# Kernel optimization log

Hardware: AMD Instinct MI355X
Metric: run time of the kernel (lower is better)

The kernel has to match this reference:

```python
import jax, jax.numpy as jnp
import numpy as np

DIM = 384
K = 64               # num_classes
TEMP = 0.1
BASE_TEMP = 2.0
LAMB = 25.0
PIXEL_SIZE = 50      # pixel_update_freq * 5
K_BAN = 10
SINKHORN_ITERS = 3
BS, N = 16, 512


def _l2norm(x, eps=1e-12):
    return x / jnp.maximum(jnp.linalg.norm(x, axis=-1, keepdims=True), eps)


def _online_clustering(scores):
    # SwAV-style Sinkhorn in log space on lamb-scaled cosine logits, then argmax.
    logq = scores
    for _ in range(SINKHORN_ITERS):
        logq = logq - jax.scipy.special.logsumexp(logq, axis=1, keepdims=True)
        logq = logq - jax.scipy.special.logsumexp(logq, axis=0, keepdims=True)
    return jnp.argmax(logq, axis=1)


def _supcon(anchor, y_anchor, contrast, y_contrast, exclude_diag, require_pos):
    # mask[i,j] = 1 if same label
    mask = (y_anchor[:, None] == y_contrast[None, :]).astype(anchor.dtype)
    logits = (anchor @ contrast.T) / TEMP
    logits = logits - jax.lax.stop_gradient(jnp.max(logits, axis=1, keepdims=True))
    if exclude_diag:
        mask = mask * (1.0 - jnp.eye(anchor.shape[0], dtype=anchor.dtype))
    exp_logits = jnp.exp(logits)
    # note: neg_mask = 1 - mask, so for exclude_diag the self term counts as negative (faithful)
    neg = (exp_logits * (1.0 - mask)).sum(axis=1, keepdims=True)
    log_prob = logits - jnp.log(exp_logits + neg)
    pos_cnt = mask.sum(axis=1)
    num = (mask * log_prob).sum(axis=1)
    if require_pos:
        valid = (pos_cnt > 0).astype(anchor.dtype)
        mlpp = jnp.where(pos_cnt > 0, num / jnp.maximum(pos_cnt, 1.0), 0.0)
        return -(TEMP / BASE_TEMP) * jnp.sum(mlpp) / jnp.maximum(valid.sum(), 1.0)
    return jnp.mean(-(TEMP / BASE_TEMP) * num / pos_cnt)


def _forward(feats, off_feats, cluster_center, point_queue):
    bs, n, dim = off_feats.shape
    n_off = _l2norm(off_feats.reshape(-1, dim))
    cluster_feats = jnp.concatenate([n_off, point_queue.reshape(-1, dim)], axis=0)
    log_alpha = cluster_feats @ cluster_center.T              # (bs*n + K*PIXEL_SIZE, K)
    labels = _online_clustering(log_alpha * LAMB)[: bs * n]
    f = _l2norm(feats).reshape(-1, dim)
    # ppc2: anchors vs sampled queue entries (same random column indices for every class)
    k_samp = PIXEL_SIZE - K_BAN
    idx = jax.random.permutation(jax.random.key(1), PIXEL_SIZE)[:k_samp]
    x_c = point_queue[:, idx, :].reshape(-1, dim)             # (K*k_samp, dim)
    y_c = jnp.repeat(jnp.arange(K), k_samp)
    loss = _supcon(f, labels, x_c, y_c, exclude_diag=False, require_pos=False)
    # ppc: anchors vs anchors, diagonal removed from positives
    loss = loss + _supcon(f, labels, f, labels, exclude_diag=True, require_pos=True)
    return loss


def setup_inputs() -> dict:
    key = jax.random.key(0)
    k1, k2, k3, k4 = jax.random.split(key, 4)
    feats = jax.random.normal(k1, (BS, N, DIM), dtype=jnp.float32)
    off_feats = jax.random.normal(k2, (BS, N, DIM), dtype=jnp.float32)
    cluster_center = _l2norm(jax.random.normal(k3, (K, DIM), dtype=jnp.float32))
    point_queue = _l2norm(jax.random.normal(k4, (K, PIXEL_SIZE, DIM), dtype=jnp.float32))
    return {"feats": feats, "off_feats": off_feats,
            "cluster_center": cluster_center, "point_queue": point_queue}


def reference(feats, off_feats, cluster_center, point_queue):
    return _forward(feats, off_feats, cluster_center, point_queue)
```

## Files before the change

### kernel.cpp

```cpp
#include <hip/hip_runtime.h>
#include <stdint.h>
#include <algorithm>

#define DIM   384
#define KCLS  64
#define NPIX  50
#define KSAMP 40
#define NANCH 8192
#define NQ    3200
#define NTOT  11392
#define NXC   2560

typedef __attribute__((ext_vector_type(8)))  short s16x8;
typedef __attribute__((ext_vector_type(16))) float f32x16;

struct Idx40 { int v[KSAMP]; };

__device__ __forceinline__ float wave_sum64(float v){
  #pragma unroll
  for (int o = 32; o >= 1; o >>= 1) v += __shfl_xor(v, o);
  return v;
}

__device__ __forceinline__ unsigned short f2bf(float x){
  union { float f; uint32_t u; } c; c.f = x;
  uint32_t r = c.u + 0x7FFFu + ((c.u >> 16) & 1u);
  if ((c.u & 0x7F800000u) == 0x7F800000u) r = c.u;
  return (unsigned short)(r >> 16);
}

__device__ __forceinline__ float bf2f(unsigned short h){
  union { uint32_t u; float f; } c; c.u = ((uint32_t)h) << 16;
  return c.f;
}

__device__ __forceinline__ void split_hl(float x, unsigned short& hi, unsigned short& lo){
  hi = f2bf(x);
  lo = f2bf(x - bf2f(hi));
}

__device__ __forceinline__ void gload16(const unsigned short* g, unsigned short* l){
  __builtin_amdgcn_global_load_lds(
      (const __attribute__((address_space(1))) unsigned int*)g,
      (__attribute__((address_space(3))) unsigned int*)l, 16, 0, 0);
}

__global__ __launch_bounds__(256) void norm_copy_k(const float* __restrict__ feats,
    const float* __restrict__ off, const float* __restrict__ pq,
    const float* __restrict__ CC,
    unsigned short* __restrict__ fNh,
    unsigned short* __restrict__ CFhi, unsigned short* __restrict__ CFlo,
    unsigned short* __restrict__ cchi, unsigned short* __restrict__ cclo,
    unsigned short* __restrict__ xch, Idx40 idx){
  int row  = blockIdx.x * 4 + (threadIdx.x >> 6);
  int lane = threadIdx.x & 63;
  if (row < 2 * NANCH){
    const float* src = (row < NANCH) ? feats + (size_t)row * DIM
                                     : off + (size_t)(row - NANCH) * DIM;
    float v[6]; float ss = 0.f;
    #pragma unroll
    for (int e = 0; e < 6; e++){ v[e] = src[lane + 64 * e]; ss += v[e] * v[e]; }
    ss = wave_sum64(ss);
    float inv = 1.f / fmaxf(sqrtf(ss), 1e-12f);
    if (row < NANCH){
      unsigned short* dh = fNh + (size_t)row * DIM;
      #pragma unroll
      for (int e = 0; e < 6; e++) dh[lane + 64 * e] = f2bf(v[e] * inv);
    } else {
      size_t base = (size_t)(row - NANCH) * DIM;
      #pragma unroll
      for (int e = 0; e < 6; e++){
        unsigned short h, l;
        split_hl(v[e] * inv, h, l);
        CFhi[base + lane + 64 * e] = h;
        CFlo[base + lane + 64 * e] = l;
      }
    }
  } else if (row < 2 * NANCH + NQ){
    int q = row - 2 * NANCH;
    const float* src = pq + (size_t)q * DIM;
    size_t base = (size_t)(NANCH + q) * DIM;
    #pragma unroll
    for (int e = 0; e < 6; e++){
      unsigned short h, l;
      split_hl(src[lane + 64 * e], h, l);
      CFhi[base + lane + 64 * e] = h;
      CFlo[base + lane + 64 * e] = l;
    }
  } else if (row < 2 * NANCH + NQ + KCLS){
    int r = row - 2 * NANCH - NQ;
    size_t base = (size_t)r * DIM;
    #pragma unroll
    for (int e = 0; e < 6; e++){
      unsigned short h, l;
      split_hl(CC[base + lane + 64 * e], h, l);
      cchi[base + lane + 64 * e] = h;
      cclo[base + lane + 64 * e] = l;
    }
  } else {
    int q = row - 2 * NANCH - NQ - KCLS;
    int c = q / KSAMP, t = q - c * KSAMP;
    const float* src = pq + ((size_t)c * NPIX + idx.v[t]) * DIM;
    unsigned short* dst = xch + (size_t)q * DIM;
    #pragma unroll
    for (int e = 0; e < 6; e++) dst[lane + 64 * e] = f2bf(src[lane + 64 * e]);
  }
}

__global__ __launch_bounds__(256) void gemm_logq_mfma_k(
    const unsigned short* __restrict__ Ahi, const unsigned short* __restrict__ Alo,
    const unsigned short* __restrict__ Bhi, const unsigned short* __restrict__ Blo,
    float* __restrict__ logq){
  __shared__ unsigned short lAh[128 * 64], lAl[128 * 64];
  __shared__ unsigned short lBh[64 * 64],  lBl[64 * 64];
  int t = threadIdx.x;
  int lane = t & 63, w = t >> 6;
  int l31 = lane & 31, half = lane >> 5;
  int i0 = blockIdx.x * 128;

  int rA = w * 32 + l31;
  int swA = ((rA & 7) << 4);
  int rB0 = l31, rB1 = 32 + l31;
  int swB = ((l31 & 7) << 4);

  f32x16 acc0, acc1;
  #pragma unroll
  for (int r = 0; r < 16; r++){ acc0[r] = 0.f; acc1[r] = 0.f; }

  for (int kc = 0; kc < 6; kc++){
    __syncthreads();
    #pragma unroll
    for (int p = 0; p < 4; p++){
      int c = t + p * 256;
      int row = c >> 3, col = c & 7;
      int sw = ((col << 4) ^ ((row & 7) << 4));
      *(s16x8*)((char*)lAh + row * 128 + sw) =
          *(const s16x8*)(Ahi + (size_t)(i0 + row) * DIM + kc * 64 + col * 8);
      *(s16x8*)((char*)lAl + row * 128 + sw) =
          *(const s16x8*)(Alo + (size_t)(i0 + row) * DIM + kc * 64 + col * 8);
    }
    #pragma unroll
    for (int p = 0; p < 2; p++){
      int c = t + p * 256;
      int row = c >> 3, col = c & 7;
      int sw = ((col << 4) ^ ((row & 7) << 4));
      *(s16x8*)((char*)lBh + row * 128 + sw) =
          *(const s16x8*)(Bhi + (size_t)row * DIM + kc * 64 + col * 8);
      *(s16x8*)((char*)lBl + row * 128 + sw) =
          *(const s16x8*)(Blo + (size_t)row * DIM + kc * 64 + col * 8);
    }
    __syncthreads();
    #pragma unroll
    for (int kk = 0; kk < 4; kk++){
      int kb = kk * 32 + half * 16;
      s16x8 fah  = *(const s16x8*)((char*)lAh + rA * 128 + (kb ^ swA));
      s16x8 fal  = *(const s16x8*)((char*)lAl + rA * 128 + (kb ^ swA));
      s16x8 fb0h = *(const s16x8*)((char*)lBh + rB0 * 128 + (kb ^ swB));
      s16x8 fb0l = *(const s16x8*)((char*)lBl + rB0 * 128 + (kb ^ swB));
      s16x8 fb1h = *(const s16x8*)((char*)lBh + rB1 * 128 + (kb ^ swB));
      s16x8 fb1l = *(const s16x8*)((char*)lBl + rB1 * 128 + (kb ^ swB));
      acc0 = __builtin_amdgcn_mfma_f32_32x32x16_bf16(fah, fb0h, acc0, 0, 0, 0);
      acc0 = __builtin_amdgcn_mfma_f32_32x32x16_bf16(fah, fb0l, acc0, 0, 0, 0);
      acc0 = __builtin_amdgcn_mfma_f32_32x32x16_bf16(fal, fb0h, acc0, 0, 0, 0);
      acc1 = __builtin_amdgcn_mfma_f32_32x32x16_bf16(fah, fb1h, acc1, 0, 0, 0);
      acc1 = __builtin_amdgcn_mfma_f32_32x32x16_bf16(fah, fb1l, acc1, 0, 0, 0);
      acc1 = __builtin_amdgcn_mfma_f32_32x32x16_bf16(fal, fb1h, acc1, 0, 0, 0);
    }
  }
  #pragma unroll
  for (int r = 0; r < 16; r++){
    int rowp = (r & 3) + 8 * (r >> 2) + 4 * half;
    size_t row = (size_t)(i0 + w * 32 + rowp);
    logq[row * KCLS + l31]      = 25.f * acc0[r];
    logq[row * KCLS + 32 + l31] = 25.f * acc1[r];
  }
}

__global__ __launch_bounds__(256) void rowcol_k(float* __restrict__ logq,
    const float* __restrict__ csPrev, float* __restrict__ csNext, int useCol){
  int r0 = blockIdx.x * 128;
  int t = threadIdx.x, lane = t & 63, grp = t >> 6;
  float cl = useCol ? logf(csPrev[lane]) : 0.f;
  float colacc = 0.f;
  for (int r = grp; r < 128; r += 4){
    size_t off = (size_t)(r0 + r) * KCLS + lane;
    float v = logq[off] - cl;
    float m = v;
    #pragma unroll
    for (int o = 32; o >= 1; o >>= 1) m = fmaxf(m, __shfl_xor(m, o));
    float e = expf(v - m);
    float s = wave_sum64(e);
    float nv = v - (m + logf(s));
    logq[off] = nv;
    colacc += expf(nv);
  }
  __shared__ float red[4][64];
  red[grp][lane] = colacc;
  __syncthreads();
  if (t < 64) atomicAdd(&csNext[t], red[0][t] + red[1][t] + red[2][t] + red[3][t]);
}

__global__ __launch_bounds__(256) void argmax_k(const float* __restrict__ logq,
    const float* __restrict__ cs, int* __restrict__ labels, int* __restrict__ cnt){
  __shared__ float clog[KCLS];
  int t = threadIdx.x;
  if (t < KCLS) clog[t] = logf(cs[t]);
  __syncthreads();
  int i = blockIdx.x * 256 + t;
  if (i >= NANCH) return;
  float best = -INFINITY; int bj = 0;
  for (int j = 0; j < KCLS; j++){
    float v = logq[(size_t)i * KCLS + j] - clog[j];
    if (v > best){ best = v; bj = j; }
  }
  labels[i] = bj;
  atomicAdd(&cnt[bj], 1);
}

__global__ void scan_k(const int* cnt, int* offs, int* offw){
  if (threadIdx.x == 0){
    int acc = 0;
    for (int c = 0; c < KCLS; c++){ offs[c] = acc; offw[c] = acc; acc += cnt[c]; }
  }
}

__global__ __launch_bounds__(256) void scatter_k(const int* __restrict__ labels,
    int* offw, int* __restrict__ sorted, const float* __restrict__ S,
    const float* __restrict__ S2, float* __restrict__ Sp, float* __restrict__ S2p){
  int i = blockIdx.x * 256 + threadIdx.x;
  if (i >= NANCH) return;
  int p = atomicAdd(&offw[labels[i]], 1);
  sorted[p] = i;
  Sp[p]  = S[i];
  S2p[p] = S2[i];
}

__global__ __launch_bounds__(256) void sortrows_k(const unsigned short* __restrict__ fNh,
    const int* __restrict__ sorted, unsigned short* __restrict__ fNs){
  int p = blockIdx.x * 4 + (threadIdx.x >> 6);
  int lane = threadIdx.x & 63;
  int src = sorted[p];
  const uint32_t* s = (const uint32_t*)(fNh + (size_t)src * DIM);
  uint32_t* d = (uint32_t*)(fNs + (size_t)p * DIM);
  #pragma unroll
  for (int e = 0; e < 3; e++) d[lane + 64 * e] = s[lane + 64 * e];
}

__global__ __launch_bounds__(256) void rowsums2_k(
    const unsigned short* __restrict__ A, const unsigned short* __restrict__ Bself,
    const unsigned short* __restrict__ Bxc, float* __restrict__ S, float* __restrict__ S2){
  int bi = blockIdx.x;
  const unsigned short* Bp; float* dst;
  int bj0, njt; bool selfpart;
  if (blockIdx.y < 16){
    selfpart = true; Bp = Bself; dst = S;
    bj0 = bi + (int)blockIdx.y * 4;
    njt = 64 - bj0;
    if (njt <= 0) return;
    if (njt > 4) njt = 4;
  } else {
    selfpart = false; Bp = Bxc; dst = S2;
    bj0 = ((int)blockIdx.y - 16) * 4;
    njt = 4;
  }

  __shared__ unsigned short lA[128 * 64];
  __shared__ unsigned short lB[128 * 64];
  int t = threadIdx.x, lane = t & 63, w = t >> 6;
  int wr = w >> 1, wc = w & 1;
  int l31 = lane & 31, half = lane >> 5;
  int i0 = bi * 128;
  int lrow = lane >> 3, srcslot = (lane & 7) ^ lrow;
  size_t loff = (size_t)lrow * DIM + srcslot * 8;

  int rA0 = wr * 64 + l31, rA1 = rA0 + 32;
  int rB0 = wc * 64 + l31, rB1 = rB0 + 32;
  int swA = ((rA0 & 7) << 4), swB = ((rB0 & 7) << 4);

  f32x16 s0, s1, a00, a01, a10, a11;
  #pragma unroll
  for (int r = 0; r < 16; r++){ s0[r] = 0.f; s1[r] = 0.f; }

  int total = njt * 6;
  for (int s = 0; s < total; s++){
    int jt = s / 6, kc = s - jt * 6;
    int j0 = (bj0 + jt) * 128;
    __syncthreads();
    #pragma unroll
    for (int c = 0; c < 4; c++){
      int chunk = w * 4 + c;
      gload16(A  + (size_t)(i0 + chunk * 8) * DIM + kc * 64 + loff, &lA[chunk * 512]);
      gload16(Bp + (size_t)(j0 + chunk * 8) * DIM + kc * 64 + loff, &lB[chunk * 512]);
    }
    __syncthreads();
    if (kc == 0){
      #pragma unroll
      for (int r = 0; r < 16; r++){ a00[r] = 0.f; a01[r] = 0.f; a10[r] = 0.f; a11[r] = 0.f; }
    }
    const char* bA = (const char*)lA;
    const char* bB = (const char*)lB;
    #pragma unroll
    for (int kk = 0; kk < 4; kk++){
      int kb = kk * 32 + half * 16;
      s16x8 fa0 = *(const s16x8*)(bA + rA0 * 128 + (kb ^ swA));
      s16x8 fa1 = *(const s16x8*)(bA + rA1 * 128 + (kb ^ swA));
      s16x8 fb0 = *(const s16x8*)(bB + rB0 * 128 + (kb ^ swB));
      s16x8 fb1 = *(const s16x8*)(bB + rB1 * 128 + (kb ^ swB));
      a00 = __builtin_amdgcn_mfma_f32_32x32x16_bf16(fa0, fb0, a00, 0, 0, 0);
      a01 = __builtin_amdgcn_mfma_f32_32x32x16_bf16(fa0, fb1, a01, 0, 0, 0);
      a10 = __builtin_amdgcn_mfma_f32_32x32x16_bf16(fa1, fb0, a10, 0, 0, 0);
      a11 = __builtin_amdgcn_mfma_f32_32x32x16_bf16(fa1, fb1, a11, 0, 0, 0);
    }
    if (kc == 5){
      bool docol = selfpart && (bj0 + jt != bi);
      float c0 = 0.f, c1 = 0.f;
      #pragma unroll
      for (int r = 0; r < 16; r++){
        float e00 = __expf(fmaf(a00[r], 10.f, -10.f));
        float e01 = __expf(fmaf(a01[r], 10.f, -10.f));
        float e10 = __expf(fmaf(a10[r], 10.f, -10.f));
        float e11 = __expf(fmaf(a11[r], 10.f, -10.f));
        s0[r] += e00 + e01;
        s1[r] += e10 + e11;
        c0 += e00 + e10;
        c1 += e01 + e11;
      }
      if (docol){
        c0 += __shfl_xor(c0, 32);
        c1 += __shfl_xor(c1, 32);
        if (half == 0){
          atomicAdd(&dst[j0 + wc * 64 + l31], c0);
          atomicAdd(&dst[j0 + wc * 64 + 32 + l31], c1);
        }
      }
    }
  }

  #pragma unroll
  for (int o = 1; o < 32; o <<= 1){
    #pragma unroll
    for (int r = 0; r < 16; r++){
      s0[r] += __shfl_xor(s0[r], o);
      s1[r] += __shfl_xor(s1[r], o);
    }
  }
  if (l31 == 0){
    #pragma unroll
    for (int r = 0; r < 16; r++){
      int rowp = (r & 3) + 8 * (r >> 2) + 4 * half;
      atomicAdd(&dst[i0 + wr * 64 + rowp], s0[r]);
      atomicAdd(&dst[i0 + wr * 64 + 32 + rowp], s1[r]);
    }
  }
}

__device__ __forceinline__ void gram2(const s16x8* afr,
    const unsigned short* b0, const unsigned short* b1, f32x16& acc0, f32x16& acc1){
  #pragma unroll
  for (int ks = 0; ks < 24; ks++){
    s16x8 v0 = *(const s16x8*)(b0 + ks * 16);
    s16x8 v1 = *(const s16x8*)(b1 + ks * 16);
    acc0 = __builtin_amdgcn_mfma_f32_32x32x16_bf16(afr[ks], v0, acc0, 0, 0, 0);
    acc1 = __builtin_amdgcn_mfma_f32_32x32x16_bf16(afr[ks], v1, acc1, 0, 0, 0);
  }
}

__global__ __launch_bounds__(64) void classpair_k(
    const unsigned short* __restrict__ fNs, const unsigned short* __restrict__ xch,
    const int* __restrict__ offs, const int* __restrict__ cnt,
    const float* __restrict__ S, const float* __restrict__ S2,
    float* __restrict__ num2A, float* __restrict__ mlppA, float* __restrict__ validA){
  int c = blockIdx.x;
  int n = cnt[c], o0 = offs[c];
  if (n == 0) return;
  int lane = threadIdx.x;
  int l31 = lane & 31, half = lane >> 5;
  int ntiles = (n + 31) >> 5;

  for (int rt = blockIdx.y; rt < ntiles; rt += gridDim.y){
    int rpos = rt * 32 + l31;
    const unsigned short* arow = fNs + (size_t)(o0 + (rpos < n ? rpos : 0)) * DIM + half * 8;
    s16x8 afr[24];
    #pragma unroll
    for (int ks = 0; ks < 24; ks++) afr[ks] = *(const s16x8*)(arow + ks * 16);

    f32x16 p20, p21;
    #pragma unroll
    for (int r = 0; r < 16; r++){ p20[r] = 0.f; p21[r] = 0.f; }
    {
      int c1 = 32 + l31;
      const unsigned short* b0 = xch + ((size_t)c * KSAMP + l31) * DIM + half * 8;
      const unsigned short* b1 = xch + ((size_t)c * KSAMP + (c1 < KSAMP ? c1 : 0)) * DIM + half * 8;
      gram2(afr, b0, b1, p20, p21);
    }
    f32x16 red;
    #pragma unroll
    for (int r = 0; r < 16; r++){
      float v0 = expf(fmaf(p20[r], 10.f, -10.f));
      float v1 = (l31 < 8) ? expf(fmaf(p21[r], 10.f, -10.f)) : 0.f;
      red[r] = v0 + v1;
    }
    #pragma unroll
    for (int o = 1; o < 32; o <<= 1)
      #pragma unroll
      for (int r = 0; r < 16; r++) red[r] += __shfl_xor(red[r], o);
    float neg2[16];
    #pragma unroll
    for (int r = 0; r < 16; r++){
      int rowp = (r & 3) + 8 * (r >> 2) + 4 * half;
      int rp = rt * 32 + rowp;
      neg2[r] = (rp < n) ? S2[o0 + rp] - red[r] : 1.f;
    }
    #pragma unroll
    for (int r = 0; r < 16; r++){
      float l0 = fmaf(p20[r], 10.f, -10.f);
      float l1 = fmaf(p21[r], 10.f, -10.f);
      float a = l0 - logf(expf(l0) + neg2[r]);
      float b = (l31 < 8) ? l1 - logf(expf(l1) + neg2[r]) : 0.f;
      red[r] = a + b;
    }
    #pragma unroll
    for (int o = 1; o < 32; o <<= 1)
      #pragma unroll
      for (int r = 0; r < 16; r++) red[r] += __shfl_xor(red[r], o);
    if (l31 == 0){
      #pragma unroll
      for (int r = 0; r < 16; r++){
        int rowp = (r & 3) + 8 * (r >> 2) + 4 * half;
        int rp = rt * 32 + rowp;
        if (rp < n) num2A[o0 + rp] = red[r];
      }
    }

    f32x16 pe;
    #pragma unroll
    for (int r = 0; r < 16; r++) pe[r] = 0.f;
    for (int ct = 0; ct < ntiles; ct += 2){
      int cp0 = ct * 32 + l31;
      int cp1 = (ct + 1) * 32 + l31;
      bool has1 = (ct + 1) < ntiles;
      const unsigned short* b0 = fNs + (size_t)(o0 + (cp0 < n ? cp0 : 0)) * DIM + half * 8;
      const unsigned short* b1 = fNs + (size_t)(o0 + (has1 && cp1 < n ? cp1 : 0)) * DIM + half * 8;
      f32x16 a0, a1;
      #pragma unroll
      for (int r = 0; r < 16; r++){ a0[r] = 0.f; a1[r] = 0.f; }
      gram2(afr, b0, b1, a0, a1);
      #pragma unroll
      for (int r = 0; r < 16; r++){
        int rowp = (r & 3) + 8 * (r >> 2) + 4 * half;
        int rp = rt * 32 + rowp;
        if (cp0 < n && cp0 != rp) pe[r] += expf(fmaf(a0[r], 10.f, -10.f));
        if (has1 && cp1 < n && cp1 != rp) pe[r] += expf(fmaf(a1[r], 10.f, -10.f));
      }
    }
    #pragma unroll
    for (int o = 1; o < 32; o <<= 1)
      #pragma unroll
      for (int r = 0; r < 16; r++) pe[r] += __shfl_xor(pe[r], o);
    float neg[16];
    #pragma unroll
    for (int r = 0; r < 16; r++){
      int rowp = (r & 3) + 8 * (r >> 2) + 4 * half;
      int rp = rt * 32 + rowp;
      neg[r] = (rp < n) ? S[o0 + rp] - pe[r] : 1.f;
    }

    f32x16 nm;
    #pragma unroll
    for (int r = 0; r < 16; r++) nm[r] = 0.f;
    for (int ct = 0; ct < ntiles; ct += 2){
      int cp0 = ct * 32 + l31;
      int cp1 = (ct + 1) * 32 + l31;
      bool has1 = (ct + 1) < ntiles;
      const unsigned short* b0 = fNs + (size_t)(o0 + (cp0 < n ? cp0 : 0)) * DIM + half * 8;
      const unsigned short* b1 = fNs + (size_t)(o0 + (has1 && cp1 < n ? cp1 : 0)) * DIM + half * 8;
      f32x16 a0, a1;
      #pragma unroll
      for (int r = 0; r < 16; r++){ a0[r] = 0.f; a1[r] = 0.f; }
      gram2(afr, b0, b1, a0, a1);
      #pragma unroll
      for (int r = 0; r < 16; r++){
        int rowp = (r & 3) + 8 * (r >> 2) + 4 * half;
        int rp = rt * 32 + rowp;
        if (cp0 < n && cp0 != rp){
          float l = fmaf(a0[r], 10.f, -10.f);
          nm[r] += l - logf(expf(l) + neg[r]);
        }
        if (has1 && cp1 < n && cp1 != rp){
          float l = fmaf(a1[r], 10.f, -10.f);
          nm[r] += l - logf(expf(l) + neg[r]);
        }
      }
    }
    #pragma unroll
    for (int o = 1; o < 32; o <<= 1)
      #pragma unroll
      for (int r = 0; r < 16; r++) nm[r] += __shfl_xor(nm[r], o);
    if (l31 == 0){
      #pragma unroll
      for (int r = 0; r < 16; r++){
        int rowp = (r & 3) + 8 * (r >> 2) + 4 * half;
        int rp = rt * 32 + rowp;
        if (rp < n){
          if (n > 1){ mlppA[o0 + rp] = nm[r] / (float)(n - 1); validA[o0 + rp] = 1.f; }
          else      { mlppA[o0 + rp] = 0.f; validA[o0 + rp] = 0.f; }
        }
      }
    }
  }
}

__global__ __launch_bounds__(256) void finalize_k(const float* __restrict__ num2A,
    const float* __restrict__ mlppA, const float* __restrict__ validA,
    float* __restrict__ out){
  int t = threadIdx.x;
  float s2 = 0.f, sm = 0.f, sv = 0.f;
  for (int i = t; i < NANCH; i += 256){ s2 += num2A[i]; sm += mlppA[i]; sv += validA[i]; }
  __shared__ float a2[256], am[256], av[256];
  a2[t] = s2; am[t] = sm; av[t] = sv; __syncthreads();
  for (int o = 128; o >= 1; o >>= 1){
    if (t < o){ a2[t] += a2[t+o]; am[t] += am[t+o]; av[t] += av[t+o]; }
    __syncthreads();
  }
  if (t == 0){
    float loss1 = -0.05f * a2[0] / (40.f * (float)NANCH);
    float loss2 = -0.05f * am[0] / fmaxf(av[0], 1.f);
    out[0] = loss1 + loss2;
  }
}

static void tf2x32(uint32_t k0, uint32_t k1, uint32_t x0, uint32_t x1, uint32_t out[2]){
  uint32_t ks[3] = { k0, k1, k0 ^ k1 ^ 0x1BD11BDAu };
  static const int R[2][4] = { {13,15,26,6}, {17,29,16,24} };
  x0 += ks[0]; x1 += ks[1];
  for (int i = 0; i < 5; i++){
    for (int j = 0; j < 4; j++){
      x0 += x1;
      int r = R[i & 1][j];
      x1 = (x1 << r) | (x1 >> (32 - r));
      x1 ^= x0;
    }
    x0 += ks[(i + 1) % 3];
    x1 += ks[(i + 2) % 3] + (uint32_t)(i + 1);
  }
  out[0] = x0; out[1] = x1;
}

static void compute_idx(int idx_out[KSAMP]){
  uint32_t p0[2], p1[2];
  tf2x32(0u, 1u, 0u, 2u, p0);
  tf2x32(0u, 1u, 1u, 3u, p1);
  uint32_t sk0 = p0[1], sk1 = p1[1];
  uint32_t bits[NPIX];
  for (int i = 0; i < 25; i++){
    uint32_t o[2];
    tf2x32(sk0, sk1, (uint32_t)i, (uint32_t)(25 + i), o);
    bits[i] = o[0]; bits[25 + i] = o[1];
  }
  int perm[NPIX];
  for (int i = 0; i < NPIX; i++) perm[i] = i;
  std::stable_sort(perm, perm + NPIX, [&](int a, int b){ return bits[a] < bits[b]; });
  for (int i = 0; i < KSAMP; i++) idx_out[i] = perm[i];
}

extern "C" void kernel_launch(void* const* d_in, const int* in_sizes, int n_in,
                              void* d_out, int out_size, void* d_ws, size_t ws_size,
                              hipStream_t stream){
  const float* feats = (const float*)d_in[0];
  const float* off   = (const float*)d_in[1];
  const float* cc    = (const float*)d_in[2];
  const float* pq    = (const float*)d_in[3];
  float* out = (float*)d_out;

  char* ws = (char*)d_ws;
  size_t ofs = 0;
  auto alloc = [&](size_t bytes) -> void* {
    ofs = (ofs + 255) & ~(size_t)255;
    void* p = ws + ofs;
    ofs += bytes;
    return p;
  };
  float* logq   = (float*)alloc((size_t)NTOT * KCLS * 4);
  unsigned short* fNh  = (unsigned short*)alloc((size_t)NANCH * DIM * 2);
  unsigned short* fNs  = (unsigned short*)alloc((size_t)NANCH * DIM * 2);
  unsigned short* CFhi = (unsigned short*)alloc((size_t)NTOT * DIM * 2);
  unsigned short* CFlo = (unsigned short*)alloc((size_t)NTOT * DIM * 2);
  unsigned short* cchi = (unsigned short*)alloc((size_t)KCLS * DIM * 2);
  unsigned short* cclo = (unsigned short*)alloc((size_t)KCLS * DIM * 2);
  unsigned short* xch  = (unsigned short*)alloc((size_t)NXC * DIM * 2);
  float* S2     = (float*)alloc((2 * NANCH + KCLS + 3 * KCLS) * 4);
  float* S      = S2 + NANCH;
  int*   cnt    = (int*)(S2 + 2 * NANCH);
  float* cs0    = S2 + 2 * NANCH + KCLS;
  float* cs1    = cs0 + KCLS;
  float* cs2    = cs1 + KCLS;
  float* Sp     = (float*)alloc(NANCH * 4);
  float* S2p    = (float*)alloc(NANCH * 4);
  float* num2A  = (float*)alloc(NANCH * 4);
  float* mlppA  = (float*)alloc(NANCH * 4);
  float* validA = (float*)alloc(NANCH * 4);
  int* labels   = (int*)alloc(NANCH * 4);
  int* sorted   = (int*)alloc(NANCH * 4);
  int* offs     = (int*)alloc(KCLS * 4);
  int* offw     = (int*)alloc(KCLS * 4);

  Idx40 idx;
  compute_idx(idx.v);

  hipMemsetAsync(S2, 0, (2 * NANCH + 4 * KCLS) * 4, stream);
  norm_copy_k<<<(2 * NANCH + NQ + KCLS + NXC) / 4, 256, 0, stream>>>(
      feats, off, pq, cc, fNh, CFhi, CFlo, cchi, cclo, xch, idx);
  rowsums2_k<<<dim3(64, 21), 256, 0, stream>>>(fNh, fNh, xch, S, S2);
  gemm_logq_mfma_k<<<NTOT / 128, 256, 0, stream>>>(CFhi, CFlo, cchi, cclo, logq);
  rowcol_k<<<NTOT / 128, 256, 0, stream>>>(logq, cs0, cs0, 0);
  rowcol_k<<<NTOT / 128, 256, 0, stream>>>(logq, cs0, cs1, 1);
  rowcol_k<<<NTOT / 128, 256, 0, stream>>>(logq, cs1, cs2, 1);
  argmax_k<<<NANCH / 256, 256, 0, stream>>>(logq, cs2, labels, cnt);
  scan_k<<<1, 64, 0, stream>>>(cnt, offs, offw);
  scatter_k<<<NANCH / 256, 256, 0, stream>>>(labels, offw, sorted, S, S2, Sp, S2p);
  sortrows_k<<<NANCH / 4, 256, 0, stream>>>(fNh, sorted, fNs);
  classpair_k<<<dim3(KCLS, 8), 64, 0, stream>>>(fNs, xch, offs, cnt, Sp, S2p,
                                                num2A, mlppA, validA);
  finalize_k<<<1, 256, 0, stream>>>(num2A, mlppA, validA, out);
}
```

Measured before the change: 297.7 us.

## Flatten rowsums tile grid to one tile per block and shrink rowcol blocks

```diff
diff --git a/kernel.cpp b/kernel.cpp
--- a/kernel.cpp
+++ b/kernel.cpp
@@ -10,6 +10,8 @@
 #define NQ    3200
 #define NTOT  11392
 #define NXC   2560
+#define NSELFP 2080
+#define NXCT  1280
 
 typedef __attribute__((ext_vector_type(8)))  short s16x8;
 typedef __attribute__((ext_vector_type(16))) float f32x16;
@@ -178,11 +180,12 @@
 
 __global__ __launch_bounds__(256) void rowcol_k(float* __restrict__ logq,
     const float* __restrict__ csPrev, float* __restrict__ csNext, int useCol){
-  int r0 = blockIdx.x * 128;
-  int t = threadIdx.x, lane = t & 63, grp = t >> 6;
+  int r0 = blockIdx.x * 16;
+  int t = threadIdx.x, lane = t & 63, w = t >> 6;
   float cl = useCol ? logf(csPrev[lane]) : 0.f;
   float colacc = 0.f;
-  for (int r = grp; r < 128; r += 4){
+  #pragma unroll
+  for (int r = w; r < 16; r += 4){
     size_t off = (size_t)(r0 + r) * KCLS + lane;
     float v = logq[off] - cl;
     float m = v;
@@ -190,12 +193,11 @@
     for (int o = 32; o >= 1; o >>= 1) m = fmaxf(m, __shfl_xor(m, o));
     float e = expf(v - m);
     float s = wave_sum64(e);
-    float nv = v - (m + logf(s));
-    logq[off] = nv;
-    colacc += expf(nv);
+    logq[off] = v - (m + logf(s));
+    colacc += e / s;
   }
   __shared__ float red[4][64];
-  red[grp][lane] = colacc;
+  red[w][lane] = colacc;
   __syncthreads();
   if (t < 64) atomicAdd(&csNext[t], red[0][t] + red[1][t] + red[2][t] + red[3][t]);
 }
@@ -247,21 +249,26 @@
 }
 
 __global__ __launch_bounds__(256) void rowsums2_k(
-    const unsigned short* __restrict__ A, const unsigned short* __restrict__ Bself,
-    const unsigned short* __restrict__ Bxc, float* __restrict__ S, float* __restrict__ S2){
-  int bi = blockIdx.x;
+    const unsigned short* __restrict__ A, const unsigned short* __restrict__ Bxc,
+    float* __restrict__ S, float* __restrict__ S2){
+  int id = blockIdx.x;
   const unsigned short* Bp; float* dst;
-  int bj0, njt; bool selfpart;
-  if (blockIdx.y < 16){
-    selfpart = true; Bp = Bself; dst = S;
-    bj0 = bi + (int)blockIdx.y * 4;
-    njt = 64 - bj0;
-    if (njt <= 0) return;
-    if (njt > 4) njt = 4;
+  int bi, j0; bool docol;
+  if (id < NSELFP){
+    float disc = 16641.f - 8.f * (float)id;
+    int b = (int)((129.f - sqrtf(disc)) * 0.5f);
+    while (64 * b - b * (b - 1) / 2 > id) b--;
+    while (64 * (b + 1) - (b + 1) * b / 2 <= id) b++;
+    bi = b;
+    int bj = bi + (id - (64 * bi - bi * (bi - 1) / 2));
+    Bp = A; dst = S; j0 = bj * 128;
+    docol = (bj != bi);
   } else {
-    selfpart = false; Bp = Bxc; dst = S2;
-    bj0 = ((int)blockIdx.y - 16) * 4;
-    njt = 4;
+    int id2 = id - NSELFP;
+    bi = id2 / 20;
+    int bjx = id2 - bi * 20;
+    Bp = Bxc; dst = S2; j0 = bjx * 128;
+    docol = false;
   }
 
   __shared__ unsigned short lA[128 * 64];
@@ -277,14 +284,11 @@
   int rB0 = wc * 64 + l31, rB1 = rB0 + 32;
   int swA = ((rA0 & 7) << 4), swB = ((rB0 & 7) << 4);
 
-  f32x16 s0, s1, a00, a01, a10, a11;
-  #pragma unroll
-  for (int r = 0; r < 16; r++){ s0[r] = 0.f; s1[r] = 0.f; }
-
-  int total = njt * 6;
-  for (int s = 0; s < total; s++){
-    int jt = s / 6, kc = s - jt * 6;
-    int j0 = (bj0 + jt) * 128;
+  f32x16 a00, a01, a10, a11;
+  #pragma unroll
+  for (int r = 0; r < 16; r++){ a00[r] = 0.f; a01[r] = 0.f; a10[r] = 0.f; a11[r] = 0.f; }
+
+  for (int kc = 0; kc < 6; kc++){
     __syncthreads();
     #pragma unroll
     for (int c = 0; c < 4; c++){
@@ -293,10 +297,6 @@
       gload16(Bp + (size_t)(j0 + chunk * 8) * DIM + kc * 64 + loff, &lB[chunk * 512]);
     }
     __syncthreads();
-    if (kc == 0){
-      #pragma unroll
-      for (int r = 0; r < 16; r++){ a00[r] = 0.f; a01[r] = 0.f; a10[r] = 0.f; a11[r] = 0.f; }
-    }
     const char* bA = (const char*)lA;
     const char* bB = (const char*)lB;
     #pragma unroll
@@ -311,31 +311,29 @@
       a10 = __builtin_amdgcn_mfma_f32_32x32x16_bf16(fa1, fb0, a10, 0, 0, 0);
       a11 = __builtin_amdgcn_mfma_f32_32x32x16_bf16(fa1, fb1, a11, 0, 0, 0);
     }
-    if (kc == 5){
-      bool docol = selfpart && (bj0 + jt != bi);
-      float c0 = 0.f, c1 = 0.f;
-      #pragma unroll
-      for (int r = 0; r < 16; r++){
-        float e00 = __expf(fmaf(a00[r], 10.f, -10.f));
-        float e01 = __expf(fmaf(a01[r], 10.f, -10.f));
-        float e10 = __expf(fmaf(a10[r], 10.f, -10.f));
-        float e11 = __expf(fmaf(a11[r], 10.f, -10.f));
-        s0[r] += e00 + e01;
-        s1[r] += e10 + e11;
-        c0 += e00 + e10;
-        c1 += e01 + e11;
-      }
-      if (docol){
-        c0 += __shfl_xor(c0, 32);
-        c1 += __shfl_xor(c1, 32);
-        if (half == 0){
-          atomicAdd(&dst[j0 + wc * 64 + l31], c0);
-          atomicAdd(&dst[j0 + wc * 64 + 32 + l31], c1);
-        }
-      }
-    }
-  }
-
+  }
+
+  f32x16 s0, s1;
+  float c0 = 0.f, c1 = 0.f;
+  #pragma unroll
+  for (int r = 0; r < 16; r++){
+    float e00 = __expf(fmaf(a00[r], 10.f, -10.f));
+    float e01 = __expf(fmaf(a01[r], 10.f, -10.f));
+    float e10 = __expf(fmaf(a10[r], 10.f, -10.f));
+    float e11 = __expf(fmaf(a11[r], 10.f, -10.f));
+    s0[r] = e00 + e01;
+    s1[r] = e10 + e11;
+    c0 += e00 + e10;
+    c1 += e01 + e11;
+  }
+  if (docol){
+    c0 += __shfl_xor(c0, 32);
+    c1 += __shfl_xor(c1, 32);
+    if (half == 0){
+      atomicAdd(&dst[j0 + wc * 64 + l31], c0);
+      atomicAdd(&dst[j0 + wc * 64 + 32 + l31], c1);
+    }
+  }
   #pragma unroll
   for (int o = 1; o < 32; o <<= 1){
     #pragma unroll
@@ -610,11 +608,11 @@
   hipMemsetAsync(S2, 0, (2 * NANCH + 4 * KCLS) * 4, stream);
   norm_copy_k<<<(2 * NANCH + NQ + KCLS + NXC) / 4, 256, 0, stream>>>(
       feats, off, pq, cc, fNh, CFhi, CFlo, cchi, cclo, xch, idx);
-  rowsums2_k<<<dim3(64, 21), 256, 0, stream>>>(fNh, fNh, xch, S, S2);
+  rowsums2_k<<<NSELFP + NXCT, 256, 0, stream>>>(fNh, xch, S, S2);
   gemm_logq_mfma_k<<<NTOT / 128, 256, 0, stream>>>(CFhi, CFlo, cchi, cclo, logq);
-  rowcol_k<<<NTOT / 128, 256, 0, stream>>>(logq, cs0, cs0, 0);
-  rowcol_k<<<NTOT / 128, 256, 0, stream>>>(logq, cs0, cs1, 1);
-  rowcol_k<<<NTOT / 128, 256, 0, stream>>>(logq, cs1, cs2, 1);
+  rowcol_k<<<NTOT / 16, 256, 0, stream>>>(logq, cs0, cs0, 0);
+  rowcol_k<<<NTOT / 16, 256, 0, stream>>>(logq, cs0, cs1, 1);
+  rowcol_k<<<NTOT / 16, 256, 0, stream>>>(logq, cs1, cs2, 1);
   argmax_k<<<NANCH / 256, 256, 0, stream>>>(logq, cs2, labels, cnt);
   scan_k<<<1, 64, 0, stream>>>(cnt, offs, offw);
   scatter_k<<<NANCH / 256, 256, 0, stream>>>(labels, offw, sorted, S, S2, Sp, S2p);
```

Result: slower. 306.0 us (+2.8%).
